# Optimization experiments

Hardware: AMD Instinct MI355X
Metric: run time of the kernel (lower is better)

## Reference

```python
import jax, jax.numpy as jnp
import numpy as np

UNITS = 1024
NUM_HEADS = 16
MASK_VALUE = -1e12


def setup_inputs() -> dict:
    key = jax.random.key(0)
    k1, k2, k3, k4 = jax.random.split(key, 4)
    B, S = 8, 1024
    memory = jax.random.normal(k1, (B, S, 2 * UNITS), dtype=jnp.float32)
    query = jax.random.normal(k2, (B, S, UNITS), dtype=jnp.float32)
    b = jax.random.normal(k3, (S,), dtype=jnp.float32)
    seq_len = jax.random.randint(k4, (B, 1), 0, S, dtype=jnp.int32)
    return {"memory": memory, "query": query, "b": b, "seq_len": seq_len}


def _split_heads(x, n):
    # [B, S, D] -> [B, n, S, D/n]
    B, S, D = x.shape
    return x.reshape(B, S, n, D // n).transpose(0, 2, 1, 3)


def reference(memory, query, b, seq_len):
    B, S, _ = query.shape
    dh = UNITS // NUM_HEADS
    k_mem, v_mem = jnp.split(memory, 2, axis=2)
    Q = _split_heads(query, NUM_HEADS) * (dh ** -0.5)   # [B,H,S,dh]
    Kh = _split_heads(k_mem, NUM_HEADS)                  # [B,H,S,dh]
    Vh = _split_heads(v_mem, NUM_HEADS)                  # [B,H,S,dh]
    logits = jnp.einsum('bhqd,bhkd->bhqk', Q, Kh) + b    # bias broadcast over keys
    # mask: one_hot(seq_len) -> cumsum -> 1-cumsum == (pos < seq_len)
    valid = (jnp.arange(S)[None, :] < seq_len[:, 0:1]).astype(jnp.float32)  # [B,S]
    logits = logits + MASK_VALUE * (1.0 - valid)[:, None, None, :]
    weights = jax.nn.softmax(logits, axis=-1)
    out = jnp.einsum('bhqk,bhkd->bhqd', weights, Vh)
    return out.transpose(0, 2, 1, 3).reshape(B, S, UNITS)
```

## Files before the change

kernel.cpp:

```cpp
#include <hip/hip_runtime.h>

#define S_      1024
#define H_      16
#define DH      64
#define UNITS_  1024
#define MSTRIDE 2048
#define KVB     64
#define QTB     64
#define LOG2E   1.4426950408889634f

typedef __attribute__((ext_vector_type(8))) short bf16x8;
typedef __attribute__((ext_vector_type(4))) short bf16x4;
typedef __attribute__((ext_vector_type(4))) float f32x4;

__device__ __forceinline__ unsigned cvt_pk_bf16(float lo, float hi) {
    unsigned r;
    asm("v_cvt_pk_bf16_f32 %0, %1, %2" : "=v"(r) : "v"(lo), "v"(hi));
    return r;
}

#define TRD(dst, base) \
    asm volatile("ds_read_b64_tr_b16 %0, %1" : "=v"(dst) : "v"(base))
#define TRDO(dst, base, off) \
    asm volatile("ds_read_b64_tr_b16 %0, %1 offset:" #off : "=v"(dst) : "v"(base))
#define WAITL(n) \
    asm volatile("s_waitcnt lgkmcnt(" #n ")" ::: "memory"); \
    __builtin_amdgcn_sched_barrier(0)

__global__ __launch_bounds__(256, 4)
void attn_kernel(const float* __restrict__ mem, const float* __restrict__ qry,
                 const float* __restrict__ bias, const int* __restrict__ slen,
                 float* __restrict__ out)
{
    __shared__ alignas(16) unsigned short Ks[KVB][DH];
    __shared__ alignas(16) unsigned short Vs[KVB * DH];
    __shared__ alignas(16) unsigned short Pt[4][KVB][16];

    const int tid  = threadIdx.x;
    const int wq   = tid >> 6;
    const int lane = tid & 63;
    const int lr   = lane & 15;
    const int lg   = lane >> 4;

    const int b  = blockIdx.x & 7;
    const int h  = blockIdx.x >> 3;
    const int qt = blockIdx.y;

    int L = slen[b];
    if (L == 0) L = S_;
    const int ntiles = (L + KVB - 1) / KVB;

    const float* qp = qry + ((size_t)(b * S_ + qt * QTB)) * UNITS_ + h * DH;
    const float* kp = mem + ((size_t)b * S_) * MSTRIDE + h * DH;
    const float* vp = kp + UNITS_;
    float*       op = out + ((size_t)(b * S_ + qt * QTB)) * UNITS_ + h * DH;

    bf16x8 qf[2];
    #pragma unroll
    for (int kc = 0; kc < 2; ++kc) {
        const float* qrow = qp + (size_t)(wq*16 + lr) * UNITS_ + kc*32 + lg*8;
        float4 f0 = ((const float4*)qrow)[0];
        float4 f1 = ((const float4*)qrow)[1];
        const float sc = 0.125f * LOG2E;
        uint4 u;
        u.x = cvt_pk_bf16(f0.x*sc, f0.y*sc);
        u.y = cvt_pk_bf16(f0.z*sc, f0.w*sc);
        u.z = cvt_pk_bf16(f1.x*sc, f1.y*sc);
        u.w = cvt_pk_bf16(f1.z*sc, f1.w*sc);
        qf[kc] = __builtin_bit_cast(bf16x8, u);
    }

    f32x4 o[4];
    float ls4[4];
    #pragma unroll
    for (int r = 0; r < 4; ++r) { o[r] = (f32x4){0.f,0.f,0.f,0.f}; ls4[r] = 0.f; }

    const int krow = tid >> 2;
    const int dblk = tid & 3;
    const int rotb = (krow >> 2) & 3;
    const unsigned ksw0 = (unsigned)((dblk*16)     ^ ((krow & 7) * 8));
    const unsigned ksw1 = (unsigned)((dblk*16 + 8) ^ ((krow & 7) * 8));
    const int vbase = ((krow >> 2) << 8) | (dblk << 6) | ((krow & 3) << 4);
    const int r0 = (0 + rotb) & 3, r1 = (1 + rotb) & 3, r2 = (2 + rotb) & 3, r3 = (3 + rotb) & 3;

    const float* krow_p = kp + (size_t)krow * MSTRIDE + dblk * 16;
    const float* vrow_p = vp + (size_t)krow * MSTRIDE + dblk * 16;

    float4 pk0, pk1, pk2, pk3, pv0, pv1, pv2, pv3;
    {
        const float4* ksrc = (const float4*)krow_p;
        pk0 = ksrc[0]; pk1 = ksrc[1]; pk2 = ksrc[2]; pk3 = ksrc[3];
        pv0 = *(const float4*)(vrow_p + r0*4);
        pv1 = *(const float4*)(vrow_p + r1*4);
        pv2 = *(const float4*)(vrow_p + r2*4);
        pv3 = *(const float4*)(vrow_p + r3*4);
    }

    const unsigned ptw = (unsigned)(uintptr_t)&Pt[wq][0][0];
    const unsigned vsb = (unsigned)(uintptr_t)&Vs[0];
    const unsigned pa  = ptw + (unsigned)((lg*2) << 7) + (unsigned)(lr << 3);
    const unsigned va  = vsb + (unsigned)((lg*2) << 9) + (unsigned)(lr << 3);

    for (int t = 0; t < ntiles; ++t) {
        const int kvb = t * KVB;
        {
            uint4 w0, w1;
            w0.x = cvt_pk_bf16(pk0.x, pk0.y); w0.y = cvt_pk_bf16(pk0.z, pk0.w);
            w0.z = cvt_pk_bf16(pk1.x, pk1.y); w0.w = cvt_pk_bf16(pk1.z, pk1.w);
            w1.x = cvt_pk_bf16(pk2.x, pk2.y); w1.y = cvt_pk_bf16(pk2.z, pk2.w);
            w1.z = cvt_pk_bf16(pk3.x, pk3.y); w1.w = cvt_pk_bf16(pk3.z, pk3.w);
            *(uint4*)&Ks[krow][ksw0] = w0;
            *(uint4*)&Ks[krow][ksw1] = w1;
            uint2 v0, v1, v2, v3;
            v0.x = cvt_pk_bf16(pv0.x, pv0.y); v0.y = cvt_pk_bf16(pv0.z, pv0.w);
            v1.x = cvt_pk_bf16(pv1.x, pv1.y); v1.y = cvt_pk_bf16(pv1.z, pv1.w);
            v2.x = cvt_pk_bf16(pv2.x, pv2.y); v2.y = cvt_pk_bf16(pv2.z, pv2.w);
            v3.x = cvt_pk_bf16(pv3.x, pv3.y); v3.y = cvt_pk_bf16(pv3.z, pv3.w);
            *(uint2*)&Vs[vbase + r0*4] = v0;
            *(uint2*)&Vs[vbase + r1*4] = v1;
            *(uint2*)&Vs[vbase + r2*4] = v2;
            *(uint2*)&Vs[vbase + r3*4] = v3;
        }
        __syncthreads();

        if (t + 1 < ntiles) {
            const float* kn = krow_p + (size_t)(t + 1) * KVB * MSTRIDE;
            const float* vn = vrow_p + (size_t)(t + 1) * KVB * MSTRIDE;
            const float4* ksrc = (const float4*)kn;
            pk0 = ksrc[0]; pk1 = ksrc[1]; pk2 = ksrc[2]; pk3 = ksrc[3];
            pv0 = *(const float4*)(vn + r0*4);
            pv1 = *(const float4*)(vn + r1*4);
            pv2 = *(const float4*)(vn + r2*4);
            pv3 = *(const float4*)(vn + r3*4);
        }

        float bv[4];
        #pragma unroll
        for (int cb = 0; cb < 4; ++cb) {
            const int key = kvb + cb*16 + lr;
            bv[cb] = (key < L) ? bias[key] * LOG2E : -INFINITY;
        }

        __builtin_amdgcn_s_setprio(1);
        f32x4 s[4];
        #pragma unroll
        for (int cb = 0; cb < 4; ++cb) {
            f32x4 acc = (f32x4){0.f,0.f,0.f,0.f};
            #pragma unroll
            for (int kc = 0; kc < 2; ++kc) {
                bf16x8 kf = *(const bf16x8*)&Ks[cb*16 + lr][(unsigned)(kc*32 + lg*8) ^ ((unsigned)(lr & 7) * 8)];
                acc = __builtin_amdgcn_mfma_f32_16x16x32_bf16(qf[kc], kf, acc, 0, 0, 0);
            }
            s[cb] = acc;
        }
        __builtin_amdgcn_s_setprio(0);

        #pragma unroll
        for (int cb = 0; cb < 4; ++cb) {
            float e0 = exp2f(s[cb][0] + bv[cb]);
            float e1 = exp2f(s[cb][1] + bv[cb]);
            float e2 = exp2f(s[cb][2] + bv[cb]);
            float e3 = exp2f(s[cb][3] + bv[cb]);
            ls4[0] += e0; ls4[1] += e1; ls4[2] += e2; ls4[3] += e3;
            uint2 u;
            u.x = cvt_pk_bf16(e0, e1);
            u.y = cvt_pk_bf16(e2, e3);
            *(uint2*)&Pt[wq][cb*16 + lr][lg*4] = u;
        }
        asm volatile("" ::: "memory");

        {
            bf16x4 p00, p01, p10, p11;
            bf16x4 w0a, w0b, w1a, w1b, w2a, w2b, w3a, w3b;
            bf16x4 x0a, x0b, x1a, x1b, x2a, x2b, x3a, x3b;
            TRD (p00, pa);
            TRDO(p01, pa, 128);
            TRD (w0a, va);
            TRDO(w0b, va, 512);
            TRDO(w1a, va, 128);
            TRDO(w1b, va, 640);
            TRDO(w2a, va, 256);
            TRDO(w2b, va, 768);
            TRDO(w3a, va, 384);
            TRDO(w3b, va, 896);
            WAITL(6);
            TRDO(p10, pa, 1024);
            TRDO(p11, pa, 1152);
            TRDO(x0a, va, 4096);
            TRDO(x0b, va, 4608);
            TRDO(x1a, va, 4224);
            TRDO(x1b, va, 4736);
            TRDO(x2a, va, 4352);
            TRDO(x2b, va, 4864);
            TRDO(x3a, va, 4480);
            TRDO(x3b, va, 4992);
            __builtin_amdgcn_sched_barrier(0);
            __builtin_amdgcn_s_setprio(1);
            bf16x8 pf0 = __builtin_shufflevector(p00, p01, 0,1,2,3,4,5,6,7);
            o[0] = __builtin_amdgcn_mfma_f32_16x16x32_bf16(pf0, __builtin_shufflevector(w0a, w0b, 0,1,2,3,4,5,6,7), o[0], 0, 0, 0);
            WAITL(14);
            o[1] = __builtin_amdgcn_mfma_f32_16x16x32_bf16(pf0, __builtin_shufflevector(w1a, w1b, 0,1,2,3,4,5,6,7), o[1], 0, 0, 0);
            WAITL(12);
            o[2] = __builtin_amdgcn_mfma_f32_16x16x32_bf16(pf0, __builtin_shufflevector(w2a, w2b, 0,1,2,3,4,5,6,7), o[2], 0, 0, 0);
            WAITL(10);
            o[3] = __builtin_amdgcn_mfma_f32_16x16x32_bf16(pf0, __builtin_shufflevector(w3a, w3b, 0,1,2,3,4,5,6,7), o[3], 0, 0, 0);
            WAITL(6);
            bf16x8 pf1 = __builtin_shufflevector(p10, p11, 0,1,2,3,4,5,6,7);
            o[0] = __builtin_amdgcn_mfma_f32_16x16x32_bf16(pf1, __builtin_shufflevector(x0a, x0b, 0,1,2,3,4,5,6,7), o[0], 0, 0, 0);
            WAITL(4);
            o[1] = __builtin_amdgcn_mfma_f32_16x16x32_bf16(pf1, __builtin_shufflevector(x1a, x1b, 0,1,2,3,4,5,6,7), o[1], 0, 0, 0);
            WAITL(2);
            o[2] = __builtin_amdgcn_mfma_f32_16x16x32_bf16(pf1, __builtin_shufflevector(x2a, x2b, 0,1,2,3,4,5,6,7), o[2], 0, 0, 0);
            WAITL(0);
            o[3] = __builtin_amdgcn_mfma_f32_16x16x32_bf16(pf1, __builtin_shufflevector(x3a, x3b, 0,1,2,3,4,5,6,7), o[3], 0, 0, 0);
            __builtin_amdgcn_s_setprio(0);
        }
        __syncthreads();
    }

    #pragma unroll
    for (int r = 0; r < 4; ++r) {
        float v = ls4[r];
        v += __shfl_xor(v, 1, 64);
        v += __shfl_xor(v, 2, 64);
        v += __shfl_xor(v, 4, 64);
        v += __shfl_xor(v, 8, 64);
        const float inv = 1.0f / v;
        float* orow = op + (size_t)(wq*16 + lg*4 + r) * UNITS_;
        #pragma unroll
        for (int c = 0; c < 4; ++c)
            orow[c*16 + lr] = o[c][r] * inv;
    }
}

extern "C" void kernel_launch(void* const* d_in, const int* in_sizes, int n_in,
                              void* d_out, int out_size, void* d_ws, size_t ws_size,
                              hipStream_t stream) {
    const float* mem  = (const float*)d_in[0];
    const float* qry  = (const float*)d_in[1];
    const float* bias = (const float*)d_in[2];
    const int*   slen = (const int*)d_in[3];
    float*       out  = (float*)d_out;
    dim3 grid(H_ * 8, S_ / QTB, 1);
    attn_kernel<<<grid, dim3(256), 0, stream>>>(mem, qry, bias, slen, out);
}
```

Before: 213.5 us.

## Use persistent blocks with atomic work queue ordered by batch sequence length

```diff
diff --git a/kernel.cpp b/kernel.cpp
--- a/kernel.cpp
+++ b/kernel.cpp
@@ -7,6 +7,7 @@
 #define MSTRIDE 2048
 #define KVB     64
 #define QTB     64
+#define NITEMS  2048u
 #define LOG2E   1.4426950408889634f
 
 typedef __attribute__((ext_vector_type(8))) short bf16x8;
@@ -27,53 +28,40 @@
     asm volatile("s_waitcnt lgkmcnt(" #n ")" ::: "memory"); \
     __builtin_amdgcn_sched_barrier(0)
 
-__global__ __launch_bounds__(256, 4)
+__global__ void prep_kernel(const int* __restrict__ slen, unsigned* __restrict__ ws) {
+    if (threadIdx.x == 0) {
+        ws[0] = 0u;
+        int nt[8], idx[8];
+        #pragma unroll
+        for (int i = 0; i < 8; ++i) {
+            int L = slen[i]; if (L == 0) L = S_;
+            nt[i] = (L + KVB - 1) / KVB; idx[i] = i;
+        }
+        for (int i = 1; i < 8; ++i) {
+            int v = nt[i], id = idx[i], j = i - 1;
+            while (j >= 0 && nt[j] < v) { nt[j+1] = nt[j]; idx[j+1] = idx[j]; --j; }
+            nt[j+1] = v; idx[j+1] = id;
+        }
+        #pragma unroll
+        for (int i = 0; i < 8; ++i) ws[1 + i] = (unsigned)idx[i];
+    }
+}
+
+__global__ __launch_bounds__(256, 6)
 void attn_kernel(const float* __restrict__ mem, const float* __restrict__ qry,
                  const float* __restrict__ bias, const int* __restrict__ slen,
-                 float* __restrict__ out)
+                 float* __restrict__ out, unsigned* __restrict__ ws)
 {
     __shared__ alignas(16) unsigned short Ks[KVB][DH];
     __shared__ alignas(16) unsigned short Vs[KVB * DH];
     __shared__ alignas(16) unsigned short Pt[4][KVB][16];
+    __shared__ unsigned widS;
 
     const int tid  = threadIdx.x;
     const int wq   = tid >> 6;
     const int lane = tid & 63;
     const int lr   = lane & 15;
     const int lg   = lane >> 4;
-
-    const int b  = blockIdx.x & 7;
-    const int h  = blockIdx.x >> 3;
-    const int qt = blockIdx.y;
-
-    int L = slen[b];
-    if (L == 0) L = S_;
-    const int ntiles = (L + KVB - 1) / KVB;
-
-    const float* qp = qry + ((size_t)(b * S_ + qt * QTB)) * UNITS_ + h * DH;
-    const float* kp = mem + ((size_t)b * S_) * MSTRIDE + h * DH;
-    const float* vp = kp + UNITS_;
-    float*       op = out + ((size_t)(b * S_ + qt * QTB)) * UNITS_ + h * DH;
-
-    bf16x8 qf[2];
-    #pragma unroll
-    for (int kc = 0; kc < 2; ++kc) {
-        const float* qrow = qp + (size_t)(wq*16 + lr) * UNITS_ + kc*32 + lg*8;
-        float4 f0 = ((const float4*)qrow)[0];
-        float4 f1 = ((const float4*)qrow)[1];
-        const float sc = 0.125f * LOG2E;
-        uint4 u;
-        u.x = cvt_pk_bf16(f0.x*sc, f0.y*sc);
-        u.y = cvt_pk_bf16(f0.z*sc, f0.w*sc);
-        u.z = cvt_pk_bf16(f1.x*sc, f1.y*sc);
-        u.w = cvt_pk_bf16(f1.z*sc, f1.w*sc);
-        qf[kc] = __builtin_bit_cast(bf16x8, u);
-    }
-
-    f32x4 o[4];
-    float ls4[4];
-    #pragma unroll
-    for (int r = 0; r < 4; ++r) { o[r] = (f32x4){0.f,0.f,0.f,0.f}; ls4[r] = 0.f; }
 
     const int krow = tid >> 2;
     const int dblk = tid & 3;
@@ -83,153 +71,192 @@
     const int vbase = ((krow >> 2) << 8) | (dblk << 6) | ((krow & 3) << 4);
     const int r0 = (0 + rotb) & 3, r1 = (1 + rotb) & 3, r2 = (2 + rotb) & 3, r3 = (3 + rotb) & 3;
 
-    const float* krow_p = kp + (size_t)krow * MSTRIDE + dblk * 16;
-    const float* vrow_p = vp + (size_t)krow * MSTRIDE + dblk * 16;
-
-    float4 pk0, pk1, pk2, pk3, pv0, pv1, pv2, pv3;
-    {
-        const float4* ksrc = (const float4*)krow_p;
-        pk0 = ksrc[0]; pk1 = ksrc[1]; pk2 = ksrc[2]; pk3 = ksrc[3];
-        pv0 = *(const float4*)(vrow_p + r0*4);
-        pv1 = *(const float4*)(vrow_p + r1*4);
-        pv2 = *(const float4*)(vrow_p + r2*4);
-        pv3 = *(const float4*)(vrow_p + r3*4);
-    }
-
     const unsigned ptw = (unsigned)(uintptr_t)&Pt[wq][0][0];
     const unsigned vsb = (unsigned)(uintptr_t)&Vs[0];
     const unsigned pa  = ptw + (unsigned)((lg*2) << 7) + (unsigned)(lr << 3);
     const unsigned va  = vsb + (unsigned)((lg*2) << 9) + (unsigned)(lr << 3);
 
-    for (int t = 0; t < ntiles; ++t) {
-        const int kvb = t * KVB;
+    for (;;) {
+        if (tid == 0) widS = atomicAdd(&ws[0], 1u);
+        __syncthreads();
+        const unsigned wid = widS;
+        if (wid >= NITEMS) break;
+        const int b  = (int)ws[1 + (wid >> 8)];
+        const int h  = (int)((wid >> 4) & 15u);
+        const int qt = (int)(wid & 15u);
+
+        int L = slen[b];
+        if (L == 0) L = S_;
+        const int ntiles = (L + KVB - 1) / KVB;
+
+        const float* qp = qry + ((size_t)(b * S_ + qt * QTB)) * UNITS_ + h * DH;
+        const float* kp = mem + ((size_t)b * S_) * MSTRIDE + h * DH;
+        const float* vp = kp + UNITS_;
+        float*       op = out + ((size_t)(b * S_ + qt * QTB)) * UNITS_ + h * DH;
+
+        bf16x8 qf[2];
+        #pragma unroll
+        for (int kc = 0; kc < 2; ++kc) {
+            const float* qrow = qp + (size_t)(wq*16 + lr) * UNITS_ + kc*32 + lg*8;
+            float4 f0 = ((const float4*)qrow)[0];
+            float4 f1 = ((const float4*)qrow)[1];
+            const float sc = 0.125f * LOG2E;
+            uint4 u;
+            u.x = cvt_pk_bf16(f0.x*sc, f0.y*sc);
+            u.y = cvt_pk_bf16(f0.z*sc, f0.w*sc);
+            u.z = cvt_pk_bf16(f1.x*sc, f1.y*sc);
+            u.w = cvt_pk_bf16(f1.z*sc, f1.w*sc);
+            qf[kc] = __builtin_bit_cast(bf16x8, u);
+        }
+
+        f32x4 o[4];
+        float ls4[4];
+        #pragma unroll
+        for (int r = 0; r < 4; ++r) { o[r] = (f32x4){0.f,0.f,0.f,0.f}; ls4[r] = 0.f; }
+
+        const float* krow_p = kp + (size_t)krow * MSTRIDE + dblk * 16;
+        const float* vrow_p = vp + (size_t)krow * MSTRIDE + dblk * 16;
+
+        float4 pk0, pk1, pk2, pk3, pv0, pv1, pv2, pv3;
         {
-            uint4 w0, w1;
-            w0.x = cvt_pk_bf16(pk0.x, pk0.y); w0.y = cvt_pk_bf16(pk0.z, pk0.w);
-            w0.z = cvt_pk_bf16(pk1.x, pk1.y); w0.w = cvt_pk_bf16(pk1.z, pk1.w);
-            w1.x = cvt_pk_bf16(pk2.x, pk2.y); w1.y = cvt_pk_bf16(pk2.z, pk2.w);
-            w1.z = cvt_pk_bf16(pk3.x, pk3.y); w1.w = cvt_pk_bf16(pk3.z, pk3.w);
-            *(uint4*)&Ks[krow][ksw0] = w0;
-            *(uint4*)&Ks[krow][ksw1] = w1;
-            uint2 v0, v1, v2, v3;
-            v0.x = cvt_pk_bf16(pv0.x, pv0.y); v0.y = cvt_pk_bf16(pv0.z, pv0.w);
-            v1.x = cvt_pk_bf16(pv1.x, pv1.y); v1.y = cvt_pk_bf16(pv1.z, pv1.w);
-            v2.x = cvt_pk_bf16(pv2.x, pv2.y); v2.y = cvt_pk_bf16(pv2.z, pv2.w);
-            v3.x = cvt_pk_bf16(pv3.x, pv3.y); v3.y = cvt_pk_bf16(pv3.z, pv3.w);
-            *(uint2*)&Vs[vbase + r0*4] = v0;
-            *(uint2*)&Vs[vbase + r1*4] = v1;
-            *(uint2*)&Vs[vbase + r2*4] = v2;
-            *(uint2*)&Vs[vbase + r3*4] = v3;
-        }
-        __syncthreads();
-
-        if (t + 1 < ntiles) {
-            const float* kn = krow_p + (size_t)(t + 1) * KVB * MSTRIDE;
-            const float* vn = vrow_p + (size_t)(t + 1) * KVB * MSTRIDE;
-            const float4* ksrc = (const float4*)kn;
+            const float4* ksrc = (const float4*)krow_p;
             pk0 = ksrc[0]; pk1 = ksrc[1]; pk2 = ksrc[2]; pk3 = ksrc[3];
-            pv0 = *(const float4*)(vn + r0*4);
-            pv1 = *(const float4*)(vn + r1*4);
-            pv2 = *(const float4*)(vn + r2*4);
-            pv3 = *(const float4*)(vn + r3*4);
-        }
-
-        float bv[4];
-        #pragma unroll
-        for (int cb = 0; cb < 4; ++cb) {
-            const int key = kvb + cb*16 + lr;
-            bv[cb] = (key < L) ? bias[key] * LOG2E : -INFINITY;
-        }
-
-        __builtin_amdgcn_s_setprio(1);
-        f32x4 s[4];
-        #pragma unroll
-        for (int cb = 0; cb < 4; ++cb) {
-            f32x4 acc = (f32x4){0.f,0.f,0.f,0.f};
-            #pragma unroll
-            for (int kc = 0; kc < 2; ++kc) {
-                bf16x8 kf = *(const bf16x8*)&Ks[cb*16 + lr][(unsigned)(kc*32 + lg*8) ^ ((unsigned)(lr & 7) * 8)];
-                acc = __builtin_amdgcn_mfma_f32_16x16x32_bf16(qf[kc], kf, acc, 0, 0, 0);
-            }
-            s[cb] = acc;
-        }
-        __builtin_amdgcn_s_setprio(0);
-
-        #pragma unroll
-        for (int cb = 0; cb < 4; ++cb) {
-            float e0 = exp2f(s[cb][0] + bv[cb]);
-            float e1 = exp2f(s[cb][1] + bv[cb]);
-            float e2 = exp2f(s[cb][2] + bv[cb]);
-            float e3 = exp2f(s[cb][3] + bv[cb]);
-            ls4[0] += e0; ls4[1] += e1; ls4[2] += e2; ls4[3] += e3;
-            uint2 u;
-            u.x = cvt_pk_bf16(e0, e1);
-            u.y = cvt_pk_bf16(e2, e3);
-            *(uint2*)&Pt[wq][cb*16 + lr][lg*4] = u;
-        }
-        asm volatile("" ::: "memory");
-
-        {
-            bf16x4 p00, p01, p10, p11;
-            bf16x4 w0a, w0b, w1a, w1b, w2a, w2b, w3a, w3b;
-            bf16x4 x0a, x0b, x1a, x1b, x2a, x2b, x3a, x3b;
-            TRD (p00, pa);
-            TRDO(p01, pa, 128);
-            TRD (w0a, va);
-            TRDO(w0b, va, 512);
-            TRDO(w1a, va, 128);
-            TRDO(w1b, va, 640);
-            TRDO(w2a, va, 256);
-            TRDO(w2b, va, 768);
-            TRDO(w3a, va, 384);
-            TRDO(w3b, va, 896);
-            WAITL(6);
-            TRDO(p10, pa, 1024);
-            TRDO(p11, pa, 1152);
-            TRDO(x0a, va, 4096);
-            TRDO(x0b, va, 4608);
-            TRDO(x1a, va, 4224);
-            TRDO(x1b, va, 4736);
-            TRDO(x2a, va, 4352);
-            TRDO(x2b, va, 4864);
-            TRDO(x3a, va, 4480);
-            TRDO(x3b, va, 4992);
-            __builtin_amdgcn_sched_barrier(0);
+            pv0 = *(const float4*)(vrow_p + r0*4);
+            pv1 = *(const float4*)(vrow_p + r1*4);
+            pv2 = *(const float4*)(vrow_p + r2*4);
+            pv3 = *(const float4*)(vrow_p + r3*4);
+        }
+
+        for (int t = 0; t < ntiles; ++t) {
+            const int kvb = t * KVB;
+            {
+                uint4 w0, w1;
+                w0.x = cvt_pk_bf16(pk0.x, pk0.y); w0.y = cvt_pk_bf16(pk0.z, pk0.w);
+                w0.z = cvt_pk_bf16(pk1.x, pk1.y); w0.w = cvt_pk_bf16(pk1.z, pk1.w);
+                w1.x = cvt_pk_bf16(pk2.x, pk2.y); w1.y = cvt_pk_bf16(pk2.z, pk2.w);
+                w1.z = cvt_pk_bf16(pk3.x, pk3.y); w1.w = cvt_pk_bf16(pk3.z, pk3.w);
+                *(uint4*)&Ks[krow][ksw0] = w0;
+                *(uint4*)&Ks[krow][ksw1] = w1;
+                uint2 v0, v1, v2, v3;
+                v0.x = cvt_pk_bf16(pv0.x, pv0.y); v0.y = cvt_pk_bf16(pv0.z, pv0.w);
+                v1.x = cvt_pk_bf16(pv1.x, pv1.y); v1.y = cvt_pk_bf16(pv1.z, pv1.w);
+                v2.x = cvt_pk_bf16(pv2.x, pv2.y); v2.y = cvt_pk_bf16(pv2.z, pv2.w);
+                v3.x = cvt_pk_bf16(pv3.x, pv3.y); v3.y = cvt_pk_bf16(pv3.z, pv3.w);
+                *(uint2*)&Vs[vbase + r0*4] = v0;
+                *(uint2*)&Vs[vbase + r1*4] = v1;
+                *(uint2*)&Vs[vbase + r2*4] = v2;
+                *(uint2*)&Vs[vbase + r3*4] = v3;
+            }
+            __syncthreads();
+
+            if (t + 1 < ntiles) {
+                const float* kn = krow_p + (size_t)(t + 1) * KVB * MSTRIDE;
+                const float* vn = vrow_p + (size_t)(t + 1) * KVB * MSTRIDE;
+                const float4* ksrc = (const float4*)kn;
+                pk0 = ksrc[0]; pk1 = ksrc[1]; pk2 = ksrc[2]; pk3 = ksrc[3];
+                pv0 = *(const float4*)(vn + r0*4);
+                pv1 = *(const float4*)(vn + r1*4);
+                pv2 = *(const float4*)(vn + r2*4);
+                pv3 = *(const float4*)(vn + r3*4);
+            }
+
+            float bv[4];
+            #pragma unroll
+            for (int cb = 0; cb < 4; ++cb) {
+                const int key = kvb + cb*16 + lr;
+                bv[cb] = (key < L) ? bias[key] * LOG2E : -INFINITY;
+            }
+
             __builtin_amdgcn_s_setprio(1);
-            bf16x8 pf0 = __builtin_shufflevector(p00, p01, 0,1,2,3,4,5,6,7);
-            o[0] = __builtin_amdgcn_mfma_f32_16x16x32_bf16(pf0, __builtin_shufflevector(w0a, w0b, 0,1,2,3,4,5,6,7), o[0], 0, 0, 0);
-            WAITL(14);
-            o[1] = __builtin_amdgcn_mfma_f32_16x16x32_bf16(pf0, __builtin_shufflevector(w1a, w1b, 0,1,2,3,4,5,6,7), o[1], 0, 0, 0);
-            WAITL(12);
-            o[2] = __builtin_amdgcn_mfma_f32_16x16x32_bf16(pf0, __builtin_shufflevector(w2a, w2b, 0,1,2,3,4,5,6,7), o[2], 0, 0, 0);
-            WAITL(10);
-            o[3] = __builtin_amdgcn_mfma_f32_16x16x32_bf16(pf0, __builtin_shufflevector(w3a, w3b, 0,1,2,3,4,5,6,7), o[3], 0, 0, 0);
-            WAITL(6);
-            bf16x8 pf1 = __builtin_shufflevector(p10, p11, 0,1,2,3,4,5,6,7);
-            o[0] = __builtin_amdgcn_mfma_f32_16x16x32_bf16(pf1, __builtin_shufflevector(x0a, x0b, 0,1,2,3,4,5,6,7), o[0], 0, 0, 0);
-            WAITL(4);
-            o[1] = __builtin_amdgcn_mfma_f32_16x16x32_bf16(pf1, __builtin_shufflevector(x1a, x1b, 0,1,2,3,4,5,6,7), o[1], 0, 0, 0);
-            WAITL(2);
-            o[2] = __builtin_amdgcn_mfma_f32_16x16x32_bf16(pf1, __builtin_shufflevector(x2a, x2b, 0,1,2,3,4,5,6,7), o[2], 0, 0, 0);
-            WAITL(0);
-            o[3] = __builtin_amdgcn_mfma_f32_16x16x32_bf16(pf1, __builtin_shufflevector(x3a, x3b, 0,1,2,3,4,5,6,7), o[3], 0, 0, 0);
+            f32x4 s[4];
+            #pragma unroll
+            for (int cb = 0; cb < 4; ++cb) {
+                f32x4 acc = (f32x4){0.f,0.f,0.f,0.f};
+                #pragma unroll
+                for (int kc = 0; kc < 2; ++kc) {
+                    bf16x8 kf = *(const bf16x8*)&Ks[cb*16 + lr][(unsigned)(kc*32 + lg*8) ^ ((unsigned)(lr & 7) * 8)];
+                    acc = __builtin_amdgcn_mfma_f32_16x16x32_bf16(qf[kc], kf, acc, 0, 0, 0);
+                }
+                s[cb] = acc;
+            }
             __builtin_amdgcn_s_setprio(0);
-        }
-        __syncthreads();
-    }
-
-    #pragma unroll
-    for (int r = 0; r < 4; ++r) {
-        float v = ls4[r];
-        v += __shfl_xor(v, 1, 64);
-        v += __shfl_xor(v, 2, 64);
-        v += __shfl_xor(v, 4, 64);
-        v += __shfl_xor(v, 8, 64);
-        const float inv = 1.0f / v;
-        float* orow = op + (size_t)(wq*16 + lg*4 + r) * UNITS_;
-        #pragma unroll
-        for (int c = 0; c < 4; ++c)
-            orow[c*16 + lr] = o[c][r] * inv;
+
+            #pragma unroll
+            for (int cb = 0; cb < 4; ++cb) {
+                float e0 = exp2f(s[cb][0] + bv[cb]);
+                float e1 = exp2f(s[cb][1] + bv[cb]);
+                float e2 = exp2f(s[cb][2] + bv[cb]);
+                float e3 = exp2f(s[cb][3] + bv[cb]);
+                ls4[0] += e0; ls4[1] += e1; ls4[2] += e2; ls4[3] += e3;
+                uint2 u;
+                u.x = cvt_pk_bf16(e0, e1);
+                u.y = cvt_pk_bf16(e2, e3);
+                *(uint2*)&Pt[wq][cb*16 + lr][lg*4] = u;
+            }
+            asm volatile("" ::: "memory");
+
+            {
+                bf16x4 p00, p01, p10, p11;
+                bf16x4 w0a, w0b, w1a, w1b, w2a, w2b, w3a, w3b;
+                bf16x4 x0a, x0b, x1a, x1b, x2a, x2b, x3a, x3b;
+                TRD (p00, pa);
+                TRDO(p01, pa, 128);
+                TRD (w0a, va);
+                TRDO(w0b, va, 512);
+                TRDO(w1a, va, 128);
+                TRDO(w1b, va, 640);
+                TRDO(w2a, va, 256);
+                TRDO(w2b, va, 768);
+                TRDO(w3a, va, 384);
+                TRDO(w3b, va, 896);
+                WAITL(6);
+                TRDO(p10, pa, 1024);
+                TRDO(p11, pa, 1152);
+                TRDO(x0a, va, 4096);
+                TRDO(x0b, va, 4608);
+                TRDO(x1a, va, 4224);
+                TRDO(x1b, va, 4736);
+                TRDO(x2a, va, 4352);
+                TRDO(x2b, va, 4864);
+                TRDO(x3a, va, 4480);
+                TRDO(x3b, va, 4992);
+                __builtin_amdgcn_sched_barrier(0);
+                __builtin_amdgcn_s_setprio(1);
+                bf16x8 pf0 = __builtin_shufflevector(p00, p01, 0,1,2,3,4,5,6,7);
+                o[0] = __builtin_amdgcn_mfma_f32_16x16x32_bf16(pf0, __builtin_shufflevector(w0a, w0b, 0,1,2,3,4,5,6,7), o[0], 0, 0, 0);
+                WAITL(14);
+                o[1] = __builtin_amdgcn_mfma_f32_16x16x32_bf16(pf0, __builtin_shufflevector(w1a, w1b, 0,1,2,3,4,5,6,7), o[1], 0, 0, 0);
+                WAITL(12);
+                o[2] = __builtin_amdgcn_mfma_f32_16x16x32_bf16(pf0, __builtin_shufflevector(w2a, w2b, 0,1,2,3,4,5,6,7), o[2], 0, 0, 0);
+                WAITL(10);
+                o[3] = __builtin_amdgcn_mfma_f32_16x16x32_bf16(pf0, __builtin_shufflevector(w3a, w3b, 0,1,2,3,4,5,6,7), o[3], 0, 0, 0);
+                WAITL(6);
+                bf16x8 pf1 = __builtin_shufflevector(p10, p11, 0,1,2,3,4,5,6,7);
+                o[0] = __builtin_amdgcn_mfma_f32_16x16x32_bf16(pf1, __builtin_shufflevector(x0a, x0b, 0,1,2,3,4,5,6,7), o[0], 0, 0, 0);
+                WAITL(4);
+                o[1] = __builtin_amdgcn_mfma_f32_16x16x32_bf16(pf1, __builtin_shufflevector(x1a, x1b, 0,1,2,3,4,5,6,7), o[1], 0, 0, 0);
+                WAITL(2);
+                o[2] = __builtin_amdgcn_mfma_f32_16x16x32_bf16(pf1, __builtin_shufflevector(x2a, x2b, 0,1,2,3,4,5,6,7), o[2], 0, 0, 0);
+                WAITL(0);
+                o[3] = __builtin_amdgcn_mfma_f32_16x16x32_bf16(pf1, __builtin_shufflevector(x3a, x3b, 0,1,2,3,4,5,6,7), o[3], 0, 0, 0);
+                __builtin_amdgcn_s_setprio(0);
+            }
+            __syncthreads();
+        }
+
+        #pragma unroll
+        for (int r = 0; r < 4; ++r) {
+            float v = ls4[r];
+            v += __shfl_xor(v, 1, 64);
+            v += __shfl_xor(v, 2, 64);
+            v += __shfl_xor(v, 4, 64);
+            v += __shfl_xor(v, 8, 64);
+            const float inv = 1.0f / v;
+            float* orow = op + (size_t)(wq*16 + lg*4 + r) * UNITS_;
+            #pragma unroll
+            for (int c = 0; c < 4; ++c)
+                orow[c*16 + lr] = o[c][r] * inv;
+        }
     }
 }
 
@@ -241,6 +268,7 @@
     const float* bias = (const float*)d_in[2];
     const int*   slen = (const int*)d_in[3];
     float*       out  = (float*)d_out;
-    dim3 grid(H_ * 8, S_ / QTB, 1);
-    attn_kernel<<<grid, dim3(256), 0, stream>>>(mem, qry, bias, slen, out);
-}
+    unsigned*    ws   = (unsigned*)d_ws;
+    prep_kernel<<<1, 64, 0, stream>>>(slen, ws);
+    attn_kernel<<<1536, dim3(256), 0, stream>>>(mem, qry, bias, slen, out, ws);
+}
```

After: 425.6 us. +99.3%, slower.
